# Performance work log

Measured on AMD Instinct MI355X. Metric: run time of the kernel, lower is better.

Reference implementation:

```python
import jax, jax.numpy as jnp
import numpy as np

N = 100000   # nodes
E = 1600000  # edges (avg degree 16)
IN = 128     # in_channels
H = 256      # hidden_channels
L = 3        # num_layers
C = 2        # num_classes
EPS = 1e-5   # BatchNorm eps


def setup_inputs() -> dict:
    key = jax.random.key(0)
    ks = jax.random.split(key, 8)
    s = 0.05
    x = jax.random.normal(ks[0], (N, IN), jnp.float32)
    edge_index = jax.random.randint(ks[1], (2, E), 0, N)
    return dict(
        x=x,
        edge_index=edge_index,
        proj_w=jax.random.normal(ks[2], (IN, H), jnp.float32) * s,
        proj_b=jnp.zeros((H,), jnp.float32),
        lin_l_w=jax.random.normal(ks[3], (L, H, H), jnp.float32) * s,
        lin_l_b=jnp.zeros((L, H), jnp.float32),
        lin_r_w=jax.random.normal(ks[4], (L, H, H), jnp.float32) * s,
        bn_g=jnp.ones((L, H), jnp.float32),
        bn_b=jnp.zeros((L, H), jnp.float32),
        fc1_w=jax.random.normal(ks[5], (H, H // 2), jnp.float32) * s,
        fc1_b=jnp.zeros((H // 2,), jnp.float32),
        fc2_w=jax.random.normal(ks[6], (H // 2, C), jnp.float32) * s,
        fc2_b=jnp.zeros((C,), jnp.float32),
    )


def reference(x, edge_index, proj_w, proj_b, lin_l_w, lin_l_b, lin_r_w,
              bn_g, bn_b, fc1_w, fc1_b, fc2_w, fc2_b):
    src, dst = edge_index[0], edge_index[1]
    # in-degree for mean aggregation (SAGEConv aggr='mean')
    deg = jax.ops.segment_sum(jnp.ones((E,), x.dtype), dst, num_segments=N)
    inv_deg = (1.0 / jnp.maximum(deg, 1.0))[:, None]  # [N,1]

    h = jax.nn.relu(x @ proj_w + proj_b)  # [N,H]; dropout is identity in eval
    for i in range(L):
        # SAGEConv: lin_l(mean_{j in N(i)} h_j) + lin_r(h_i)
        agg = jax.ops.segment_sum(h[src], dst, num_segments=N) * inv_deg  # [N,H]
        out = agg @ lin_l_w[i] + lin_l_b[i] + h @ lin_r_w[i]
        # BatchNorm over nodes (batch statistics, biased variance)
        mu = out.mean(axis=0)
        var = out.var(axis=0)
        out = (out - mu) * jax.lax.rsqrt(var + EPS) * bn_g[i] + bn_b[i]
        out = jax.nn.relu(out)
        h = out + h if i > 0 else out  # residual from layer 1 onward

    embeddings = h
    z = jax.nn.relu(embeddings @ fc1_w + fc1_b)
    logits = z @ fc2_w + fc2_b
    return (logits, embeddings)
```

## Files before the change

### kernel.cpp

```cpp
#include <hip/hip_runtime.h>
#include <stdint.h>

#define NN 100000
#define NE 1600000
#define INC 128
#define HID 256
#define MP  100096
#define NBK 391
#define EPB 2048

typedef unsigned short u16;
typedef __attribute__((ext_vector_type(2))) float f32x2;
typedef __attribute__((ext_vector_type(4))) float f32x4;
typedef __attribute__((ext_vector_type(8))) short s16x8;

static __device__ __forceinline__ float bf2f(u16 u){
  union { uint32_t i; float f; } v; v.i = ((uint32_t)u) << 16; return v.f;
}
static __device__ __forceinline__ u16 f2bf(float f){
  union { float f; uint32_t i; } v; v.f = f;
  uint32_t r = v.i + 0x7FFFu + ((v.i >> 16) & 1u);
  return (u16)(r >> 16);
}
static __device__ __forceinline__ void up8(uint4 o, float* v){
  v[0]=bf2f((u16)(o.x&0xffffu)); v[1]=bf2f((u16)(o.x>>16));
  v[2]=bf2f((u16)(o.y&0xffffu)); v[3]=bf2f((u16)(o.y>>16));
  v[4]=bf2f((u16)(o.z&0xffffu)); v[5]=bf2f((u16)(o.z>>16));
  v[6]=bf2f((u16)(o.w&0xffffu)); v[7]=bf2f((u16)(o.w>>16));
}
static __device__ __forceinline__ uint4 pk8(const float* v){
  uint4 o;
  o.x = (uint32_t)f2bf(v[0]) | ((uint32_t)f2bf(v[1])<<16);
  o.y = (uint32_t)f2bf(v[2]) | ((uint32_t)f2bf(v[3])<<16);
  o.z = (uint32_t)f2bf(v[4]) | ((uint32_t)f2bf(v[5])<<16);
  o.w = (uint32_t)f2bf(v[6]) | ((uint32_t)f2bf(v[7])<<16);
  return o;
}
static __device__ __forceinline__ uint2 pkf8(const float* r){
  uint32_t lo = __builtin_amdgcn_cvt_pk_fp8_f32(r[0], r[1], 0u, false);
  lo = __builtin_amdgcn_cvt_pk_fp8_f32(r[2], r[3], lo, true);
  uint32_t hi = __builtin_amdgcn_cvt_pk_fp8_f32(r[4], r[5], 0u, false);
  hi = __builtin_amdgcn_cvt_pk_fp8_f32(r[6], r[7], hi, true);
  return make_uint2(lo, hi);
}

static __device__ __forceinline__ void gload16(const void* g, void* l){
  __builtin_amdgcn_global_load_lds((const __attribute__((address_space(1))) void*)g,
                                   (__attribute__((address_space(3))) void*)l, 16, 0, 0);
}


__global__ __launch_bounds__(256) void zero_k(float* bnacc, int* bcnt){
  int i = blockIdx.x*256 + threadIdx.x;
  if (i < 3*8192) bnacc[i] = 0.f;
  if (i < NBK) bcnt[i] = 0;
}

__global__ __launch_bounds__(256) void cvt_k(const float* __restrict__ src, u16* __restrict__ dst, int n4){
  int i = blockIdx.x*256 + threadIdx.x;
  if (i >= n4) return;
  float4 v = ((const float4*)src)[i];
  uint2 o;
  o.x = (uint32_t)f2bf(v.x) | ((uint32_t)f2bf(v.y)<<16);
  o.y = (uint32_t)f2bf(v.z) | ((uint32_t)f2bf(v.w)<<16);
  ((uint2*)dst)[i] = o;
}

__global__ __launch_bounds__(256) void cvt8_k(const uint4* __restrict__ h, uint2* __restrict__ h8, int n){
  int i = blockIdx.x*256 + threadIdx.x;
  if (i >= n) return;
  float v[8];
  up8(h[i], v);
  h8[i] = pkf8(v);
}

__global__ __launch_bounds__(256) void pack_k(const float* __restrict__ src, u16* __restrict__ dst,
                                              int K, int NC, int ksoff){
  int t = blockIdx.x*256 + threadIdx.x;
  if (t >= K*NC) return;
  int k = t / NC, n = t % NC;
  int NT = NC >> 4;
  int ks = ksoff + (k >> 5);
  int l  = ((k >> 3) & 3)*16 + (n & 15);
  int j  = k & 7;
  dst[((size_t)(ks*NT + (n>>4))*64 + l)*8 + j] = f2bf(src[(size_t)k*NC + n]);
}


__global__ __launch_bounds__(256) void bhist_k(const int* __restrict__ ei, int* __restrict__ bcnt){
  __shared__ int h[NBK];
  for (int i = threadIdx.x; i < NBK; i += 256) h[i] = 0;
  __syncthreads();
  int e0 = blockIdx.x * EPB;
  #pragma unroll
  for (int j = 0; j < EPB/256; ++j){
    int e = e0 + j*256 + threadIdx.x;
    if (e < NE) atomicAdd(&h[ei[NE + e] >> 8], 1);
  }
  __syncthreads();
  for (int i = threadIdx.x; i < NBK; i += 256)
    if (h[i]) atomicAdd(&bcnt[i], h[i]);
}

__global__ __launch_bounds__(512) void bscan_k(const int* __restrict__ bcnt, int* __restrict__ bcur){
  __shared__ int sd[512];
  int t = threadIdx.x;
  int v = (t < NBK) ? bcnt[t] : 0;
  sd[t] = v; __syncthreads();
  for (int o = 1; o < 512; o <<= 1){
    int x = (t >= o) ? sd[t-o] : 0;
    __syncthreads();
    sd[t] += x;
    __syncthreads();
  }
  if (t < NBK) bcur[t] = sd[t] - v;
}

__global__ __launch_bounds__(256) void bfill_k(const int* __restrict__ ei, int* __restrict__ bcur,
                                               uint2* __restrict__ epair){
  __shared__ int cnt[NBK];
  __shared__ int gb[NBK];
  for (int i = threadIdx.x; i < NBK; i += 256) cnt[i] = 0;
  __syncthreads();
  int e0 = blockIdx.x * EPB;
  int srcv[EPB/256], dstv[EPB/256], rnk[EPB/256];
  #pragma unroll
  for (int j = 0; j < EPB/256; ++j){
    int e = e0 + j*256 + threadIdx.x;
    if (e < NE){
      srcv[j] = ei[e];
      dstv[j] = ei[NE + e];
      rnk[j]  = atomicAdd(&cnt[dstv[j] >> 8], 1);
    } else dstv[j] = -1;
  }
  __syncthreads();
  for (int i = threadIdx.x; i < NBK; i += 256){
    int c = cnt[i];
    gb[i] = c ? atomicAdd(&bcur[i], c) : 0;
  }
  __syncthreads();
  #pragma unroll
  for (int j = 0; j < EPB/256; ++j){
    if (dstv[j] >= 0)
      epair[gb[dstv[j] >> 8] + rnk[j]] = make_uint2((unsigned)srcv[j], (unsigned)dstv[j]);
  }
}

__global__ __launch_bounds__(256) void csort_k(const uint2* __restrict__ epair,
                                               const int* __restrict__ bcnt, const int* __restrict__ bcur,
                                               int* __restrict__ ci, int* __restrict__ rp){
  __shared__ int hist[256], pfx[256], cnt2[256];
  int b = blockIdx.x, t = threadIdx.x;
  int cnt  = bcnt[b];
  int base = bcur[b] - cnt;
  hist[t] = 0; cnt2[t] = 0;
  __syncthreads();
  for (int e = t; e < cnt; e += 256)
    atomicAdd(&hist[epair[base + e].y & 255u], 1);
  __syncthreads();
  int v = hist[t];
  pfx[t] = v;
  __syncthreads();
  for (int o = 1; o < 256; o <<= 1){
    int x = (t >= o) ? pfx[t - o] : 0;
    __syncthreads();
    pfx[t] += x;
    __syncthreads();
  }
  int node = b*256 + t;
  if (node < NN) rp[node] = base + pfx[t] - v;
  if (b == NBK-1 && t == 0) rp[NN] = NE;
  for (int e = t; e < cnt; e += 256){
    uint2 p = epair[base + e];
    int ld = (int)(p.y & 255u);
    int r  = atomicAdd(&cnt2[ld], 1);
    ci[base + pfx[ld] - hist[ld] + r] = (int)p.x;
  }
}


__global__ __launch_bounds__(256) void agg8_k(const int* __restrict__ rp, const int* __restrict__ ci,
                                              const uint4* __restrict__ h8, u16* __restrict__ ag){
  int wid  = (int)((blockIdx.x*256u + threadIdx.x) >> 6);
  int lane = threadIdx.x & 63;
  int ql   = lane & 15;
  int w    = wid*4 + (lane >> 4);
  bool act = (w < NN);
  int e0 = 0, e1 = 0;
  if (act){ e0 = rp[w]; e1 = rp[w+1]; }
  int cnt = e1 - e0;

  float a[16];
  #pragma unroll
  for (int k = 0; k < 16; ++k) a[k] = 0.f;

  for (int base = 0; __any(base < cnt); base += 16){
    int rem = cnt - base;
    int my = 0;
    if (ql < rem) my = ci[e0 + base + ql];
    for (int j0 = 0; j0 < 16 && __any(j0 < rem); j0 += 4){
      uint4 v[4];
      #pragma unroll
      for (int jj = 0; jj < 4; ++jj){
        int j = j0 + jj;
        int s = __shfl(my, (lane & 48) + j);
        v[jj] = make_uint4(0,0,0,0);
        if (j < rem) v[jj] = h8[(size_t)s*16 + ql];
      }
      #pragma unroll
      for (int jj = 0; jj < 4; ++jj){
        uint32_t wd[4] = {v[jj].x, v[jj].y, v[jj].z, v[jj].w};
        #pragma unroll
        for (int p = 0; p < 4; ++p){
          f32x2 lo = __builtin_amdgcn_cvt_pk_f32_fp8(wd[p], false);
          f32x2 hi = __builtin_amdgcn_cvt_pk_f32_fp8(wd[p], true);
          a[p*4+0] += lo[0]; a[p*4+1] += lo[1];
          a[p*4+2] += hi[0]; a[p*4+3] += hi[1];
        }
      }
    }
  }

  if (act){
    float inv = 1.0f / (float)(cnt > 0 ? cnt : 1);
    float r0[8], r1[8];
    #pragma unroll
    for (int k = 0; k < 8; ++k){ r0[k] = a[k]*inv; r1[k] = a[8+k]*inv; }
    uint4* agu = (uint4*)ag;
    agu[(size_t)w*32 + ql*2]     = pk8(r0);
    agu[(size_t)w*32 + ql*2 + 1] = pk8(r1);
  }
}


__global__ __launch_bounds__(256) void aggb_k(const int* __restrict__ rp, const int* __restrict__ ci,
                                              const u16* __restrict__ h, u16* __restrict__ ag){
  int w = (int)((blockIdx.x*256u + threadIdx.x) >> 6);
  int lane = threadIdx.x & 63;
  if (w >= NN) return;
  int e0 = rp[w], e1 = rp[w+1];
  const uint2* hu = (const uint2*)h;
  float a0=0.f, a1=0.f, a2=0.f, a3=0.f;
  for (int base = e0; base < e1; base += 64){
    int cnt = e1 - base; if (cnt > 64) cnt = 64;
    int my = ci[base + (lane < cnt ? lane : cnt-1)];
    int i = 0;
    for (; i + 4 <= cnt; i += 4){
      int s0 = __builtin_amdgcn_readlane(my, i);
      int s1 = __builtin_amdgcn_readlane(my, i+1);
      int s2 = __builtin_amdgcn_readlane(my, i+2);
      int s3 = __builtin_amdgcn_readlane(my, i+3);
      uint2 v0 = hu[(size_t)s0*64 + lane];
      uint2 v1 = hu[(size_t)s1*64 + lane];
      uint2 v2 = hu[(size_t)s2*64 + lane];
      uint2 v3 = hu[(size_t)s3*64 + lane];
      a0 += bf2f((u16)(v0.x&0xffffu)) + bf2f((u16)(v1.x&0xffffu)) + bf2f((u16)(v2.x&0xffffu)) + bf2f((u16)(v3.x&0xffffu));
      a1 += bf2f((u16)(v0.x>>16))     + bf2f((u16)(v1.x>>16))     + bf2f((u16)(v2.x>>16))     + bf2f((u16)(v3.x>>16));
      a2 += bf2f((u16)(v0.y&0xffffu)) + bf2f((u16)(v1.y&0xffffu)) + bf2f((u16)(v2.y&0xffffu)) + bf2f((u16)(v3.y&0xffffu));
      a3 += bf2f((u16)(v0.y>>16))     + bf2f((u16)(v1.y>>16))     + bf2f((u16)(v2.y>>16))     + bf2f((u16)(v3.y>>16));
    }
    for (; i < cnt; ++i){
      int s0 = __builtin_amdgcn_readlane(my, i);
      uint2 v = hu[(size_t)s0*64 + lane];
      a0 += bf2f((u16)(v.x&0xffffu));
      a1 += bf2f((u16)(v.x>>16));
      a2 += bf2f((u16)(v.y&0xffffu));
      a3 += bf2f((u16)(v.y>>16));
    }
  }
  int d = e1 - e0;
  float inv = 1.0f / (float)(d > 0 ? d : 1);
  uint2 o;
  o.x = (uint32_t)f2bf(a0*inv) | ((uint32_t)f2bf(a1*inv) << 16);
  o.y = (uint32_t)f2bf(a2*inv) | ((uint32_t)f2bf(a3*inv) << 16);
  ((uint2*)ag)[(size_t)w*64 + lane] = o;
}


template<int TR, int KS1, int KS2, int NCC, int EPI>
__global__ __launch_bounds__(256, 3) void gemm2_k(
    const u16* __restrict__ A1, const u16* __restrict__ A2,
    const u16* __restrict__ Wp, const float* __restrict__ bias,
    u16* __restrict__ Cout, int M, float* __restrict__ stS)
{
  constexpr int NT    = NCC >> 4;
  constexpr int MF    = TR / 32;
  constexpr int NS1   = KS1 / 2;
  constexpr int NSTEP = (KS1 + KS2) / 2;

  __shared__ u16 Al[2][TR*64];
  __shared__ u16 Bl[2][2*8*64*8];

  const int t    = threadIdx.x;
  const int lane = t & 63;
  const int wv   = t >> 6;
  const int wr   = wv >> 1, wc = wv & 1;
  const int r15  = lane & 15, kg = lane >> 4;
  const int rb   = blockIdx.x * TR;
  const int nh   = blockIdx.y;
  const int nt0  = nh * 8;

  f32x4 acc[MF][4];
  #pragma unroll
  for (int m = 0; m < MF; ++m)
    #pragma unroll
    for (int n = 0; n < 4; ++n){ f32x4 z = {0.f,0.f,0.f,0.f}; acc[m][n] = z; }

  auto stage = [&](int step, int bsel){
    const bool inA1 = (step < NS1);
    const u16* Ab   = inA1 ? A1 : A2;
    const int  Krow = (inA1 ? KS1 : KS2) * 32;
    const int  kloc = (inA1 ? step : step - NS1) * 64;
    #pragma unroll
    for (int c = 0; c < TR/32; ++c){
      int row = c*32 + wv*8 + (lane >> 3);
      int gc  = (lane & 7) ^ (row & 7);
      const u16* g = Ab + (size_t)(rb + row)*Krow + kloc + gc*8;
      gload16(g, &Al[bsel][c*2048 + wv*512]);
    }
    const int s0 = step * 2;
    #pragma unroll
    for (int c = 0; c < 4; ++c){
      int base = c*4096 + wv*1024;
      int sl   = base >> 13;
      int ntl  = (base >> 10) & 7;
      const u16* g = Wp + ((size_t)((s0 + sl)*NT + nt0 + ntl)*64)*8 + lane*8;
      gload16(g, &Bl[bsel][base >> 1]);
    }
  };

  stage(0, 0);
  __syncthreads();

  #pragma unroll
  for (int step = 0; step < NSTEP; ++step){
    const int cur = step & 1;
    if (step + 1 < NSTEP) stage(step + 1, cur ^ 1);

    s16x8 af[2][MF], bf[2][4];
    const char* Ab = (const char*)&Al[cur][0];
    const char* Bb = (const char*)&Bl[cur][0];
    #pragma unroll
    for (int sl = 0; sl < 2; ++sl){
      #pragma unroll
      for (int m = 0; m < MF; ++m){
        int row = wr*(MF*16) + m*16 + r15;
        int c16 = (sl*4 + kg) ^ (row & 7);
        af[sl][m] = *(const s16x8*)(Ab + row*128 + c16*16);
      }
      #pragma unroll
      for (int n = 0; n < 4; ++n)
        bf[sl][n] = *(const s16x8*)(Bb + sl*8192 + (wc*4 + n)*1024 + lane*16);
    }
    #pragma unroll
    for (int sl = 0; sl < 2; ++sl)
      #pragma unroll
      for (int m = 0; m < MF; ++m)
        #pragma unroll
        for (int n = 0; n < 4; ++n)
          acc[m][n] = __builtin_amdgcn_mfma_f32_16x16x32_bf16(af[sl][m], bf[sl][n], acc[m][n], 0, 0, 0);

    __syncthreads();
  }

  #pragma unroll
  for (int n = 0; n < 4; ++n){
    int col = nh*128 + wc*64 + n*16 + r15;
    float bc = bias[col];
    float s = 0.f, q = 0.f;
    #pragma unroll
    for (int m = 0; m < MF; ++m){
      int rbase = rb + wr*(MF*16) + m*16 + kg*4;
      #pragma unroll
      for (int r = 0; r < 4; ++r){
        int row = rbase + r;
        float val = acc[m][n][r] + bc;
        if (EPI == 0) val = fmaxf(val, 0.f);
        bool ok = row < M;
        if (ok) Cout[(size_t)row*NCC + col] = f2bf(val);
        if (EPI == 1 && ok){ s += val; q += val*val; }
      }
    }
    if (EPI == 1){
      s += __shfl_xor(s, 16); s += __shfl_xor(s, 32);
      q += __shfl_xor(q, 16); q += __shfl_xor(q, 32);
      if (lane < 16){
        int idx = ((blockIdx.x & 15) << 9) + col;
        atomicAdd(&stS[idx], s);
        atomicAdd(&stS[idx + 256], q);
      }
    }
  }
}


__global__ __launch_bounds__(256) void bnfin_k(const float* __restrict__ acc,
                                               const float* __restrict__ g, const float* __restrict__ b,
                                               float* __restrict__ coef){
  int c = threadIdx.x;
  float s = 0.f, q = 0.f;
  #pragma unroll
  for (int j = 0; j < 16; ++j){
    s += acc[j*512 + c];
    q += acc[j*512 + 256 + c];
  }
  float mean = s * (1.0f / (float)NN);
  float var  = q * (1.0f / (float)NN) - mean*mean;
  float sc = g[c] * rsqrtf(var + 1e-5f);
  coef[c] = sc;
  coef[256 + c] = b[c] - mean*sc;
}

__global__ __launch_bounds__(256) void bnapply_k(const uint4* __restrict__ outb, uint4* __restrict__ h,
                                                 uint2* __restrict__ h8,
                                                 const float* __restrict__ coef, int layer, int wr8){
  int i = blockIdx.x*256 + threadIdx.x;
  if (i >= NN*32) return;
  int col0 = (i & 31) * 8;
  const float4* scp = (const float4*)(coef + col0);
  const float4* shp = (const float4*)(coef + 256 + col0);
  float4 s0 = scp[0], s1 = scp[1], t0 = shp[0], t1 = shp[1];
  float sc[8] = {s0.x,s0.y,s0.z,s0.w,s1.x,s1.y,s1.z,s1.w};
  float sh[8] = {t0.x,t0.y,t0.z,t0.w,t1.x,t1.y,t1.z,t1.w};
  float v[8], r[8];
  up8(outb[i], v);
  #pragma unroll
  for (int j = 0; j < 8; ++j) r[j] = fmaxf(v[j]*sc[j] + sh[j], 0.f);
  if (layer > 0){
    float hv[8];
    up8(h[i], hv);
    #pragma unroll
    for (int j = 0; j < 8; ++j) r[j] += hv[j];
  }
  h[i] = pk8(r);
  if (wr8) h8[i] = pkf8(r);
}


__global__ __launch_bounds__(256) void fc2_k(const u16* __restrict__ z, const float* __restrict__ w2,
                                             const float* __restrict__ b2, float* __restrict__ out){
  int w = (int)((blockIdx.x*256u + threadIdx.x) >> 6);
  int lane = threadIdx.x & 63;
  if (w >= NN) return;
  const uint32_t* zu = (const uint32_t*)(z + (size_t)w*128);
  uint32_t p = zu[lane];
  float z0 = bf2f((u16)(p & 0xffffu));
  float z1 = bf2f((u16)(p >> 16));
  float4 wv = ((const float4*)w2)[lane];
  float p0 = z0*wv.x + z1*wv.z;
  float p1 = z0*wv.y + z1*wv.w;
  #pragma unroll
  for (int off = 1; off < 64; off <<= 1){
    p0 += __shfl_xor(p0, off);
    p1 += __shfl_xor(p1, off);
  }
  if (lane == 0){
    out[(size_t)w*2]     = p0 + b2[0];
    out[(size_t)w*2 + 1] = p1 + b2[1];
  }
}

__global__ __launch_bounds__(256) void emb_k(const u16* __restrict__ h, float* __restrict__ out, int n4){
  int i = blockIdx.x*256 + threadIdx.x;
  if (i >= n4) return;
  uint2 v = ((const uint2*)h)[i];
  float4 o;
  o.x = bf2f((u16)(v.x & 0xffffu));
  o.y = bf2f((u16)(v.x >> 16));
  o.z = bf2f((u16)(v.y & 0xffffu));
  o.w = bf2f((u16)(v.y >> 16));
  ((float4*)out)[i] = o;
}


extern "C" void kernel_launch(void* const* d_in, const int* in_sizes, int n_in,
                              void* d_out, int out_size, void* d_ws, size_t ws_size,
                              hipStream_t stream){
  const float* x       = (const float*)d_in[0];
  const int*   ei      = (const int*)d_in[1];
  const float* proj_w  = (const float*)d_in[2];
  const float* proj_b  = (const float*)d_in[3];
  const float* lin_l_w = (const float*)d_in[4];
  const float* lin_l_b = (const float*)d_in[5];
  const float* lin_r_w = (const float*)d_in[6];
  const float* bn_g    = (const float*)d_in[7];
  const float* bn_b    = (const float*)d_in[8];
  const float* fc1_w   = (const float*)d_in[9];
  const float* fc1_b   = (const float*)d_in[10];
  const float* fc2_w   = (const float*)d_in[11];
  const float* fc2_b   = (const float*)d_in[12];
  float* out = (float*)d_out;

  char* ws = (char*)d_ws;
  size_t off = 0;
  auto alloc = [&](size_t b){ size_t o = off; off = (off + b + 255) & ~(size_t)255; return o; };

  u16* bufA    = (u16*)(ws + alloc((size_t)MP*256*2));
  u16* hbuf    = (u16*)(ws + alloc((size_t)MP*256*2));
  u16* bufC    = (u16*)(ws + alloc((size_t)MP*256*2));
  uint8_t* h8  = (uint8_t*)(ws + alloc((size_t)MP*256));
  u16* wp_proj = (u16*)(ws + alloc((size_t)4*16*64*8*2));
  u16* wp_l[3];
  for (int i = 0; i < 3; ++i) wp_l[i] = (u16*)(ws + alloc((size_t)16*16*64*8*2));
  u16* wp_fc1  = (u16*)(ws + alloc((size_t)8*8*64*8*2));
  int* rp    = (int*)(ws + alloc((size_t)(NN+1)*4));
  int* ci    = (int*)(ws + alloc((size_t)NE*4));
  int* bcnt  = (int*)(ws + alloc(NBK*4));
  int* bcur  = (int*)(ws + alloc(NBK*4));
  float* bnacc = (float*)(ws + alloc(3*8192*4));
  float* coef  = (float*)(ws + alloc(3*512*4));
  uint2* epair = (uint2*)bufC;
  (void)ws_size; (void)in_sizes; (void)n_in; (void)out_size;

  const int BFB = (NE + EPB - 1)/EPB;
  const int GX = MP/64;

  zero_k<<<96, 256, 0, stream>>>(bnacc, bcnt);

  bhist_k<<<BFB, 256, 0, stream>>>(ei, bcnt);
  bscan_k<<<1, 512, 0, stream>>>(bcnt, bcur);
  bfill_k<<<BFB, 256, 0, stream>>>(ei, bcur, epair);
  csort_k<<<NBK, 256, 0, stream>>>(epair, bcnt, bcur, ci, rp);

  cvt_k<<<(NN*INC/4 + 255)/256, 256, 0, stream>>>(x, bufA, NN*INC/4);
  pack_k<<<(128*256 + 255)/256, 256, 0, stream>>>(proj_w, wp_proj, 128, 256, 0);
  for (int i = 0; i < 3; ++i){
    pack_k<<<(256*256 + 255)/256, 256, 0, stream>>>(lin_l_w + (size_t)i*65536, wp_l[i], 256, 256, 0);
    pack_k<<<(256*256 + 255)/256, 256, 0, stream>>>(lin_r_w + (size_t)i*65536, wp_l[i], 256, 256, 8);
  }
  pack_k<<<(256*128 + 255)/256, 256, 0, stream>>>(fc1_w, wp_fc1, 256, 128, 0);

  gemm2_k<64,4,0,256,0><<<dim3(GX,2), 256, 0, stream>>>(bufA, nullptr, wp_proj, proj_b,
                                                        hbuf, NN, nullptr);
  cvt8_k<<<(NN*32 + 255)/256, 256, 0, stream>>>((const uint4*)hbuf, (uint2*)h8, NN*32);

  for (int i = 0; i < 3; ++i){
    if (i < 2)
      agg8_k<<<((NN + 3)/4*64 + 255)/256, 256, 0, stream>>>(rp, ci, (const uint4*)h8, bufA);
    else
      aggb_k<<<(NN + 3)/4, 256, 0, stream>>>(rp, ci, hbuf, bufA);
    gemm2_k<64,8,8,256,1><<<dim3(GX,2), 256, 0, stream>>>(bufA, hbuf, wp_l[i], lin_l_b + (size_t)i*256,
                                                          bufC, NN, bnacc + i*8192);
    bnfin_k<<<1, 256, 0, stream>>>(bnacc + i*8192, bn_g + (size_t)i*256, bn_b + (size_t)i*256, coef + i*512);
    bnapply_k<<<(NN*32 + 255)/256, 256, 0, stream>>>((const uint4*)bufC, (uint4*)hbuf, (uint2*)h8,
                                                     coef + i*512, i, (i == 0) ? 1 : 0);
  }

  gemm2_k<64,8,0,128,0><<<dim3(GX,1), 256, 0, stream>>>(hbuf, nullptr, wp_fc1, fc1_b,
                                                        bufA, NN, nullptr);
  fc2_k<<<(NN + 3)/4, 256, 0, stream>>>(bufA, fc2_w, fc2_b, out);
  emb_k<<<(NN*64 + 255)/256, 256, 0, stream>>>(hbuf, out + 200000, NN*64);
}
```

Baseline: 779.3 us.

## Compute full output width per block with weights streamed directly into registers

The GEMM kernel now has each block cover all output columns for 64 rows, where before the columns were split across two blocks in the grid's y dimension. The activation tile is read once instead of twice. Weight fragments are no longer staged through shared memory; each wave loads its own column slice from global memory straight into registers, double-buffered per k-substep. This removes the LDS traffic and footprint for B, but each wave now issues direct global loads for weights (likely L2-served) and holds more accumulators, which raises register pressure.

```diff
diff --git a/kernel.cpp b/kernel.cpp
--- a/kernel.cpp
+++ b/kernel.cpp
@@ -277,100 +277,91 @@
 }
 
 
-template<int TR, int KS1, int KS2, int NCC, int EPI>
-__global__ __launch_bounds__(256, 3) void gemm2_k(
+template<int KS1, int KS2, int NCC, int EPI>
+__global__ __launch_bounds__(256, 3) void gemm3_k(
     const u16* __restrict__ A1, const u16* __restrict__ A2,
     const u16* __restrict__ Wp, const float* __restrict__ bias,
     u16* __restrict__ Cout, int M, float* __restrict__ stS)
 {
   constexpr int NT    = NCC >> 4;
-  constexpr int MF    = TR / 32;
+  constexpr int NFRAG = NCC / 64;
   constexpr int NS1   = KS1 / 2;
   constexpr int NSTEP = (KS1 + KS2) / 2;
 
-  __shared__ u16 Al[2][TR*64];
-  __shared__ u16 Bl[2][2*8*64*8];
+  __shared__ u16 Al[2][64*64];
 
   const int t    = threadIdx.x;
   const int lane = t & 63;
   const int wv   = t >> 6;
-  const int wr   = wv >> 1, wc = wv & 1;
   const int r15  = lane & 15, kg = lane >> 4;
-  const int rb   = blockIdx.x * TR;
-  const int nh   = blockIdx.y;
-  const int nt0  = nh * 8;
-
-  f32x4 acc[MF][4];
-  #pragma unroll
-  for (int m = 0; m < MF; ++m)
-    #pragma unroll
-    for (int n = 0; n < 4; ++n){ f32x4 z = {0.f,0.f,0.f,0.f}; acc[m][n] = z; }
-
-  auto stage = [&](int step, int bsel){
+  const int rb   = blockIdx.x * 64;
+  const int nt0w = wv * NFRAG;
+
+  f32x4 acc[4][NFRAG];
+  #pragma unroll
+  for (int m = 0; m < 4; ++m)
+    #pragma unroll
+    for (int n = 0; n < NFRAG; ++n){ f32x4 z = {0.f,0.f,0.f,0.f}; acc[m][n] = z; }
+
+  auto stageA = [&](int step, int bsel){
     const bool inA1 = (step < NS1);
     const u16* Ab   = inA1 ? A1 : A2;
     const int  Krow = (inA1 ? KS1 : KS2) * 32;
     const int  kloc = (inA1 ? step : step - NS1) * 64;
     #pragma unroll
-    for (int c = 0; c < TR/32; ++c){
+    for (int c = 0; c < 2; ++c){
       int row = c*32 + wv*8 + (lane >> 3);
       int gc  = (lane & 7) ^ (row & 7);
       const u16* g = Ab + (size_t)(rb + row)*Krow + kloc + gc*8;
       gload16(g, &Al[bsel][c*2048 + wv*512]);
     }
-    const int s0 = step * 2;
-    #pragma unroll
-    for (int c = 0; c < 4; ++c){
-      int base = c*4096 + wv*1024;
-      int sl   = base >> 13;
-      int ntl  = (base >> 10) & 7;
-      const u16* g = Wp + ((size_t)((s0 + sl)*NT + nt0 + ntl)*64)*8 + lane*8;
-      gload16(g, &Bl[bsel][base >> 1]);
-    }
   };
-
-  stage(0, 0);
+  auto loadB = [&](int ss, s16x8* dst){
+    const u16* g = Wp + ((size_t)(ss*NT + nt0w)*64 + lane)*8;
+    #pragma unroll
+    for (int n = 0; n < NFRAG; ++n)
+      dst[n] = *(const s16x8*)(g + (size_t)n*512);
+  };
+
+  s16x8 bb[2][NFRAG];
+  stageA(0, 0);
+  loadB(0, bb[0]);
   __syncthreads();
 
   #pragma unroll
   for (int step = 0; step < NSTEP; ++step){
     const int cur = step & 1;
-    if (step + 1 < NSTEP) stage(step + 1, cur ^ 1);
-
-    s16x8 af[2][MF], bf[2][4];
-    const char* Ab = (const char*)&Al[cur][0];
-    const char* Bb = (const char*)&Bl[cur][0];
+    if (step + 1 < NSTEP) stageA(step + 1, cur ^ 1);
     #pragma unroll
     for (int sl = 0; sl < 2; ++sl){
+      const int ss = step*2 + sl;
+      const int p  = ss & 1;
+      if (ss + 1 < NSTEP*2) loadB(ss + 1, bb[p ^ 1]);
+      s16x8 af[4];
+      const char* Ab = (const char*)&Al[cur][0];
       #pragma unroll
-      for (int m = 0; m < MF; ++m){
-        int row = wr*(MF*16) + m*16 + r15;
+      for (int m = 0; m < 4; ++m){
+        int row = m*16 + r15;
         int c16 = (sl*4 + kg) ^ (row & 7);
-        af[sl][m] = *(const s16x8*)(Ab + row*128 + c16*16);
+        af[m] = *(const s16x8*)(Ab + row*128 + c16*16);
       }
       #pragma unroll
-      for (int n = 0; n < 4; ++n)
-        bf[sl][n] = *(const s16x8*)(Bb + sl*8192 + (wc*4 + n)*1024 + lane*16);
-    }
-    #pragma unroll
-    for (int sl = 0; sl < 2; ++sl)
-      #pragma unroll
-      for (int m = 0; m < MF; ++m)
+      for (int m = 0; m < 4; ++m)
         #pragma unroll
-        for (int n = 0; n < 4; ++n)
-          acc[m][n] = __builtin_amdgcn_mfma_f32_16x16x32_bf16(af[sl][m], bf[sl][n], acc[m][n], 0, 0, 0);
-
+        for (int n = 0; n < NFRAG; ++n)
+          acc[m][n] = __builtin_amdgcn_mfma_f32_16x16x32_bf16(af[m], bb[p][n], acc[m][n], 0, 0, 0);
+    }
     __syncthreads();
   }
 
   #pragma unroll
-  for (int n = 0; n < 4; ++n){
-    int col = nh*128 + wc*64 + n*16 + r15;
+  for (int n = 0; n < NFRAG; ++n){
+    int col = (nt0w + n)*16 + r15;
     float bc = bias[col];
     float s = 0.f, q = 0.f;
     #pragma unroll
-    for (int m = 0; m < MF; ++m){
-      int rbase = rb + wr*(MF*16) + m*16 + kg*4;
+    for (int m = 0; m < 4; ++m){
+      int rbase = rb + m*16 + kg*4;
       #pragma unroll
       for (int r = 0; r < 4; ++r){
         int row = rbase + r;
@@ -530,8 +521,8 @@
   }
   pack_k<<<(256*128 + 255)/256, 256, 0, stream>>>(fc1_w, wp_fc1, 256, 128, 0);
 
-  gemm2_k<64,4,0,256,0><<<dim3(GX,2), 256, 0, stream>>>(bufA, nullptr, wp_proj, proj_b,
-                                                        hbuf, NN, nullptr);
+  gemm3_k<4,0,256,0><<<GX, 256, 0, stream>>>(bufA, nullptr, wp_proj, proj_b,
+                                             hbuf, NN, nullptr);
   cvt8_k<<<(NN*32 + 255)/256, 256, 0, stream>>>((const uint4*)hbuf, (uint2*)h8, NN*32);
 
   for (int i = 0; i < 3; ++i){
@@ -539,15 +530,15 @@
       agg8_k<<<((NN + 3)/4*64 + 255)/256, 256, 0, stream>>>(rp, ci, (const uint4*)h8, bufA);
     else
       aggb_k<<<(NN + 3)/4, 256, 0, stream>>>(rp, ci, hbuf, bufA);
-    gemm2_k<64,8,8,256,1><<<dim3(GX,2), 256, 0, stream>>>(bufA, hbuf, wp_l[i], lin_l_b + (size_t)i*256,
-                                                          bufC, NN, bnacc + i*8192);
+    gemm3_k<8,8,256,1><<<GX, 256, 0, stream>>>(bufA, hbuf, wp_l[i], lin_l_b + (size_t)i*256,
+                                               bufC, NN, bnacc + i*8192);
     bnfin_k<<<1, 256, 0, stream>>>(bnacc + i*8192, bn_g + (size_t)i*256, bn_b + (size_t)i*256, coef + i*512);
     bnapply_k<<<(NN*32 + 255)/256, 256, 0, stream>>>((const uint4*)bufC, (uint4*)hbuf, (uint2*)h8,
                                                      coef + i*512, i, (i == 0) ? 1 : 0);
   }
 
-  gemm2_k<64,8,0,128,0><<<dim3(GX,1), 256, 0, stream>>>(hbuf, nullptr, wp_fc1, fc1_b,
-                                                        bufA, NN, nullptr);
+  gemm3_k<8,0,128,0><<<GX, 256, 0, stream>>>(hbuf, nullptr, wp_fc1, fc1_b,
+                                             bufA, NN, nullptr);
   fc2_k<<<(NN + 3)/4, 256, 0, stream>>>(bufA, fc2_w, fc2_b, out);
   emb_k<<<(NN*64 + 255)/256, 256, 0, stream>>>(hbuf, out + 200000, NN*64);
 }
```

Result: faster. 692.2 us (-11.2%).
